# Optimization experiments

Hardware: AMD Instinct MI355X
Metric: run time of the kernel (lower is better)

The kernel has to match this reference:

```python
import jax, jax.numpy as jnp
import numpy as np

BIT = 64
NUM_TRAIN = 200000
BATCH = 256
NUM_CLASSES = 100
MAX_SAMPLE = 30          # max_SampleNum in original
ALPHA = 0.01             # config['alpha']
M = 2 * BIT              # self.m = 2 * bit


def setup_inputs() -> dict:
    key = jax.random.key(0)
    k1, k2, k3, k4, k5 = jax.random.split(key, 5)
    u = jax.random.normal(k1, (BATCH, BIT), dtype=jnp.float32)
    y = jax.random.randint(k2, (BATCH,), 0, NUM_CLASSES)
    # distinct scatter targets into the bank, like dataloader sample indices
    ind = jax.random.choice(k3, NUM_TRAIN, (BATCH,), replace=False)
    U = jax.random.normal(k4, (NUM_TRAIN, BIT), dtype=jnp.float32)
    Y = jax.random.randint(k5, (NUM_TRAIN,), 0, NUM_CLASSES).astype(jnp.float32)
    return {"u": u, "y": y, "ind": ind, "U": U, "Y": Y}


def reference(u, y, ind, U, Y):
    yf = y.astype(jnp.float32)
    # scatter update of the memory bank (u.data -> detached in original)
    U = U.at[ind].set(jax.lax.stop_gradient(u))
    Y = Y.at[ind].set(yf)

    # For each sample, the first MAX_SAMPLE ascending indices with Y == y[i]
    # (same as torch.where(self.Y == indx)[0][:max_SampleNum]).
    match = (Y[None, :] == yf[:, None])                       # (B, N)
    pos = jnp.arange(NUM_TRAIN, dtype=jnp.int32)
    # matched positions keep their index; unmatched get index + N -> sorted after
    key_mat = jnp.where(match, pos[None, :], pos[None, :] + NUM_TRAIN)  # (B, N)
    _, order = jax.lax.top_k(-key_mat, MAX_SAMPLE)            # (B, 30) ascending matched idx first
    count = jnp.minimum(match.sum(axis=1), MAX_SAMPLE)        # per-row pool size
    valid = (jnp.arange(MAX_SAMPLE)[None, :] < count[:, None]).reshape(-1)  # (B*30,)

    pool_idx = order.reshape(-1)                              # (P,) P = B*30
    U_pool = U[pool_idx]                                      # (P, bit)
    Y_pool = Y[pool_idx]                                      # (P,)

    # pairwise squared distance u vs pool
    dist = jnp.sum((u[:, None, :] - U_pool[None, :, :]) ** 2, axis=2)  # (B, P)
    mism = (yf[:, None] != Y_pool[None, :]).astype(jnp.float32)        # (B, P)
    pair = (1.0 - mism) * 0.5 * dist + mism * 0.5 * jnp.clip(M - dist, 0.0)

    vmask = valid.astype(jnp.float32)[None, :]
    step = jnp.sum(valid.astype(jnp.float32))                 # dynamic pool length in original
    loss1 = jnp.sum(pair * vmask) / (u.shape[0] * step)       # == loss.mean() over (B, step)
    loss2 = ALPHA * jnp.mean(jnp.abs(jnp.abs(u) - 1.0))
    return loss1 + loss2
```

## Files before the change

### kernel.cpp

```cpp
#include <hip/hip_runtime.h>

#define NTRAIN 200000
#define NB     256
#define BIT    64
#define MAXS   30
#define NCLS   100
#define ESPL   8
#define EPB    4
#define CHUNK  4096
#define PERT   16
#define NCLSB  (NCLS * ESPL)
#define MVAL   128.0f
#define ALPHA  0.01f

__global__ __launch_bounds__(256) void dsh_main_kernel(
    const float* __restrict__ u, const int* __restrict__ y,
    const int* __restrict__ ind, const float* __restrict__ U,
    const float* __restrict__ Y,
    float* __restrict__ partial, int* __restrict__ cntw)
{
    __shared__ int   addl[NB];
    __shared__ int   reml[NB];
    __shared__ float up_l[EPB * BIT];
    __shared__ int   pool[MAXS];
    __shared__ int   povr[EPB];
    __shared__ int   wsA[4], wsB[4], wsC[4];
    __shared__ float redf[4];

    const int t    = threadIdx.x;
    const int j    = blockIdx.x;
    const int lane = t & 63;
    const int wave = t >> 6;

    const int c = j >> 3;
    const int e = j & 7;
    const float cf = (float)c;

    const int myi = ind[t];
    const int myy = y[t];
    const int s0  = t * PERT;
    float4 yv0, yv1, yv2, yv3;
    {
        const float4* yp = (const float4*)(Y + s0);
        yv0 = yp[0]; yv1 = yp[1]; yv2 = yp[2]; yv3 = yp[3];
    }
    const float ybank = Y[myi];

    const bool ismem = (myy == c);
    const bool fneg  = ismem && (ybank != cf);
    const bool fpos  = (!ismem) && (ybank == cf);
    unsigned long long balm = __ballot(ismem);
    unsigned long long bala = __ballot(fneg);
    unsigned long long balr = __ballot(fpos);
    if (lane == 0) {
        wsA[wave] = (int)__popcll(balm);
        wsB[wave] = (int)__popcll(bala);
        wsC[wave] = (int)__popcll(balr);
    }
    __syncthreads();
    const int mult = wsA[0] + wsA[1] + wsA[2] + wsA[3];

    if (mult == 0) {
        if (t == 0) { partial[j] = 0.f; if (e == 0) cntw[c] = 0; }
        return;
    }

    const int nadd = wsB[0] + wsB[1] + wsB[2] + wsB[3];
    const int nrem = wsC[0] + wsC[1] + wsC[2] + wsC[3];
    int pa = 0, pr = 0;
    #pragma unroll
    for (int w = 0; w < 4; ++w) if (w < wave) { pa += wsB[w]; pr += wsC[w]; }
    const unsigned long long lm = (1ull << lane) - 1ull;
    if (fneg) addl[pa + (int)__popcll(bala & lm)] = myi;
    if (fpos) reml[pr + (int)__popcll(balr & lm)] = myi;
    __syncthreads();

    unsigned mbits = 0;
    if (yv0.x == cf) mbits |= 1u << 0;
    if (yv0.y == cf) mbits |= 1u << 1;
    if (yv0.z == cf) mbits |= 1u << 2;
    if (yv0.w == cf) mbits |= 1u << 3;
    if (yv1.x == cf) mbits |= 1u << 4;
    if (yv1.y == cf) mbits |= 1u << 5;
    if (yv1.z == cf) mbits |= 1u << 6;
    if (yv1.w == cf) mbits |= 1u << 7;
    if (yv2.x == cf) mbits |= 1u << 8;
    if (yv2.y == cf) mbits |= 1u << 9;
    if (yv2.z == cf) mbits |= 1u << 10;
    if (yv2.w == cf) mbits |= 1u << 11;
    if (yv3.x == cf) mbits |= 1u << 12;
    if (yv3.y == cf) mbits |= 1u << 13;
    if (yv3.z == cf) mbits |= 1u << 14;
    if (yv3.w == cf) mbits |= 1u << 15;
    for (int a2 = 0; a2 < nadd; ++a2) {
        unsigned rel = (unsigned)(addl[a2] - s0);
        if (rel < (unsigned)PERT) mbits |= 1u << rel;
    }
    for (int r2 = 0; r2 < nrem; ++r2) {
        unsigned rel = (unsigned)(reml[r2] - s0);
        if (rel < (unsigned)PERT) mbits &= ~(1u << rel);
    }
    const int mcnt = __popc(mbits);

    int x = mcnt;
    #pragma unroll
    for (int off = 1; off < 64; off <<= 1) {
        int v2 = __shfl_up(x, off, 64);
        if (lane >= off) x += v2;
    }
    if (lane == 63) wsA[wave] = x;
    if (t < EPB) povr[t] = -1;
    __syncthreads();
    int r = x - mcnt;
    #pragma unroll
    for (int w = 0; w < 4; ++w) if (w < wave) r += wsA[w];
    #pragma unroll
    for (int k = 0; k < PERT; ++k) {
        if ((mbits >> k) & 1u) {
            if (r < MAXS) pool[r] = s0 + k;
            ++r;
        }
    }
    int count = wsA[0] + wsA[1] + wsA[2] + wsA[3];
    __syncthreads();

    for (int base = CHUNK; base < NTRAIN && count < MAXS; base += CHUNK) {
        const int s = base + t * PERT;
        unsigned mb = 0;
        int mc = 0;
        if (s < NTRAIN) {
            const float4* yp = (const float4*)(Y + s);
            float4 a0 = yp[0], a1 = yp[1], a2v = yp[2], a3 = yp[3];
            if (a0.x == cf) mb |= 1u << 0;
            if (a0.y == cf) mb |= 1u << 1;
            if (a0.z == cf) mb |= 1u << 2;
            if (a0.w == cf) mb |= 1u << 3;
            if (a1.x == cf) mb |= 1u << 4;
            if (a1.y == cf) mb |= 1u << 5;
            if (a1.z == cf) mb |= 1u << 6;
            if (a1.w == cf) mb |= 1u << 7;
            if (a2v.x == cf) mb |= 1u << 8;
            if (a2v.y == cf) mb |= 1u << 9;
            if (a2v.z == cf) mb |= 1u << 10;
            if (a2v.w == cf) mb |= 1u << 11;
            if (a3.x == cf) mb |= 1u << 12;
            if (a3.y == cf) mb |= 1u << 13;
            if (a3.z == cf) mb |= 1u << 14;
            if (a3.w == cf) mb |= 1u << 15;
            for (int a2 = 0; a2 < nadd; ++a2) {
                unsigned rel = (unsigned)(addl[a2] - s);
                if (rel < (unsigned)PERT) mb |= 1u << rel;
            }
            for (int r2 = 0; r2 < nrem; ++r2) {
                unsigned rel = (unsigned)(reml[r2] - s);
                if (rel < (unsigned)PERT) mb &= ~(1u << rel);
            }
            mc = __popc(mb);
        }
        int xx = mc;
        #pragma unroll
        for (int off = 1; off < 64; off <<= 1) {
            int v2 = __shfl_up(xx, off, 64);
            if (lane >= off) xx += v2;
        }
        if (lane == 63) wsA[wave] = xx;
        __syncthreads();
        int rr = count + (xx - mc);
        #pragma unroll
        for (int w = 0; w < 4; ++w) if (w < wave) rr += wsA[w];
        #pragma unroll
        for (int k = 0; k < PERT; ++k) {
            if ((mb >> k) & 1u) {
                if (rr < MAXS) pool[rr] = s + k;
                ++rr;
            }
        }
        count += wsA[0] + wsA[1] + wsA[2] + wsA[3];
        __syncthreads();
    }
    const int cnt = (count < MAXS) ? count : MAXS;

    const int p0 = e * EPB;
    const int pe = (p0 + EPB < cnt) ? p0 + EPB : cnt;
    for (int k2 = p0; k2 < pe; ++k2)
        if (myi == pool[k2]) povr[k2 - p0] = t;
    __syncthreads();

    float4 ur[16];
    {
        const float4* urp = (const float4*)(u + t * BIT);
        #pragma unroll
        for (int q2 = 0; q2 < 16; ++q2) ur[q2] = urp[q2];
    }
    {
        const int pp = t >> 6;
        const int d  = t & 63;
        float v = 0.f;
        if (p0 + pp < pe) {
            const int ov = povr[pp];
            v = (ov >= 0) ? u[ov * BIT + d] : U[pool[p0 + pp] * BIT + d];
        }
        up_l[t] = v;
    }
    __syncthreads();

    const bool same = (myy == c);
    const int npool = pe - p0;
    float acc = 0.f;
    for (int pp = 0; pp < npool; ++pp) {
        const float4* up = (const float4*)(up_l + pp * BIT);
        float d0 = 0.f, d1 = 0.f, d2 = 0.f, d3 = 0.f;
        #pragma unroll
        for (int q2 = 0; q2 < 16; ++q2) {
            float4 v = up[q2];
            float a0 = ur[q2].x - v.x; d0 += a0 * a0;
            float a1 = ur[q2].y - v.y; d1 += a1 * a1;
            float a2 = ur[q2].z - v.z; d2 += a2 * a2;
            float a3 = ur[q2].w - v.w; d3 += a3 * a3;
        }
        const float dist = (d0 + d1) + (d2 + d3);
        acc += same ? dist : fmaxf(MVAL - dist, 0.f);
    }
    #pragma unroll
    for (int off = 32; off; off >>= 1) acc += __shfl_down(acc, off, 64);
    if (lane == 0) redf[wave] = acc;
    __syncthreads();
    if (t == 0) {
        partial[j] = (float)mult * (redf[0] + redf[1] + redf[2] + redf[3]);
        if (e == 0) cntw[c] = mult * cnt;
    }
}

__global__ __launch_bounds__(256) void dsh_final_kernel(
    const float* __restrict__ u,
    const float* __restrict__ partial, const int* __restrict__ cntw,
    float* __restrict__ out)
{
    const int t = threadIdx.x;
    const int lane = t & 63, wave = t >> 6;
    __shared__ float redp[4], reda[4];
    __shared__ int   redc[4];

    float p = partial[t] + partial[t + 256] + partial[t + 512];
    if (t < NCLSB - 768) p += partial[t + 768];
    int cc = (t < NCLS) ? cntw[t] : 0;

    float a = 0.f;
    #pragma unroll
    for (int k = 0; k < 16; ++k) {
        float4 v = ((const float4*)u)[t + 256 * k];
        a += fabsf(fabsf(v.x) - 1.f) + fabsf(fabsf(v.y) - 1.f)
           + fabsf(fabsf(v.z) - 1.f) + fabsf(fabsf(v.w) - 1.f);
    }
    #pragma unroll
    for (int off = 32; off; off >>= 1) {
        p  += __shfl_down(p,  off, 64);
        a  += __shfl_down(a,  off, 64);
        cc += __shfl_down(cc, off, 64);
    }
    if (lane == 0) { redp[wave] = p; reda[wave] = a; redc[wave] = cc; }
    __syncthreads();
    if (t == 0) {
        const float P = redp[0] + redp[1] + redp[2] + redp[3];
        const float A = reda[0] + reda[1] + reda[2] + reda[3];
        const int   S = redc[0] + redc[1] + redc[2] + redc[3];
        out[0] = 0.5f * P / (256.0f * (float)S)
               + ALPHA * (A * (1.0f / 16384.0f));
    }
}

extern "C" void kernel_launch(void* const* d_in, const int* in_sizes, int n_in,
                              void* d_out, int out_size, void* d_ws, size_t ws_size,
                              hipStream_t stream) {
    const float* u   = (const float*)d_in[0];
    const int*   y   = (const int*)d_in[1];
    const int*   ind = (const int*)d_in[2];
    const float* U   = (const float*)d_in[3];
    const float* Y   = (const float*)d_in[4];
    float* out = (float*)d_out;

    float* partial = (float*)d_ws;
    int*   cntw    = (int*)((char*)d_ws + 4096);

    dsh_main_kernel<<<dim3(NCLSB), dim3(256), 0, stream>>>(
        u, y, ind, U, Y, partial, cntw);
    dsh_final_kernel<<<dim3(1), dim3(256), 0, stream>>>(u, partial, cntw, out);
}
```

Before: 22.80 us.

## Fuse final reduction into main kernel via last-block atomic counters

Replaces the separate final reduction kernel with a last-block-done pattern. Each block stores its partial results, then bumps a two-level atomic counter (per-100-block octant, then a root), and the last block does the final reduction. A small prep kernel now launched before the main kernel resets the counters and computes the regularization sum, so that work leaves the serialized tail. The launch count stays at two. The intended saving is the tail latency of the single-block final kernel after the main grid. The cost is atomic traffic and relaxed memory ordering, which rests on an s_waitcnt and atomic reads for visibility.

```diff
diff --git a/kernel.cpp b/kernel.cpp
--- a/kernel.cpp
+++ b/kernel.cpp
@@ -5,19 +5,46 @@
 #define BIT    64
 #define MAXS   30
 #define NCLS   100
-#define ESPL   8
 #define EPB    4
 #define CHUNK  4096
 #define PERT   16
-#define NCLSB  (NCLS * ESPL)
+#define NCLSB  (NCLS * 8)
 #define MVAL   128.0f
 #define ALPHA  0.01f
+
+
+__global__ __launch_bounds__(256) void dsh_prep_kernel(
+    const float* __restrict__ u, int* __restrict__ oct, int* __restrict__ root,
+    float* __restrict__ regsum)
+{
+    const int t = threadIdx.x;
+    const int lane = t & 63, wave = t >> 6;
+    __shared__ float redf[4];
+
+    if (t < 8) oct[t] = 0;
+    if (t == 8) *root = 0;
+
+    float a = 0.f;
+    #pragma unroll
+    for (int k = 0; k < 16; ++k) {
+        float4 v = ((const float4*)u)[t + 256 * k];
+        a += fabsf(fabsf(v.x) - 1.f) + fabsf(fabsf(v.y) - 1.f)
+           + fabsf(fabsf(v.z) - 1.f) + fabsf(fabsf(v.w) - 1.f);
+    }
+    #pragma unroll
+    for (int off = 32; off; off >>= 1) a += __shfl_down(a, off, 64);
+    if (lane == 0) redf[wave] = a;
+    __syncthreads();
+    if (t == 0) *regsum = redf[0] + redf[1] + redf[2] + redf[3];
+}
 
 __global__ __launch_bounds__(256) void dsh_main_kernel(
     const float* __restrict__ u, const int* __restrict__ y,
     const int* __restrict__ ind, const float* __restrict__ U,
     const float* __restrict__ Y,
-    float* __restrict__ partial, int* __restrict__ cntw)
+    float* __restrict__ partial, int* __restrict__ cntw,
+    int* __restrict__ oct, int* __restrict__ root,
+    const float* __restrict__ regsum, float* __restrict__ out)
 {
     __shared__ int   addl[NB];
     __shared__ int   reml[NB];
@@ -25,7 +52,9 @@
     __shared__ int   pool[MAXS];
     __shared__ int   povr[EPB];
     __shared__ int   wsA[4], wsB[4], wsC[4];
-    __shared__ float redf[4];
+    __shared__ float redf[4], redg[4];
+    __shared__ int   redi[4];
+    __shared__ int   lastflag;
 
     const int t    = threadIdx.x;
     const int j    = blockIdx.x;
@@ -35,6 +64,9 @@
     const int c = j >> 3;
     const int e = j & 7;
     const float cf = (float)c;
+
+    float myPair = 0.f;
+    int   myCntW = (e == 0) ? 0 : -1;
 
     const int myi = ind[t];
     const int myy = y[t];
@@ -60,210 +92,217 @@
     __syncthreads();
     const int mult = wsA[0] + wsA[1] + wsA[2] + wsA[3];
 
-    if (mult == 0) {
-        if (t == 0) { partial[j] = 0.f; if (e == 0) cntw[c] = 0; }
-        return;
-    }
-
-    const int nadd = wsB[0] + wsB[1] + wsB[2] + wsB[3];
-    const int nrem = wsC[0] + wsC[1] + wsC[2] + wsC[3];
-    int pa = 0, pr = 0;
-    #pragma unroll
-    for (int w = 0; w < 4; ++w) if (w < wave) { pa += wsB[w]; pr += wsC[w]; }
-    const unsigned long long lm = (1ull << lane) - 1ull;
-    if (fneg) addl[pa + (int)__popcll(bala & lm)] = myi;
-    if (fpos) reml[pr + (int)__popcll(balr & lm)] = myi;
+    if (mult > 0) {
+        const int nadd = wsB[0] + wsB[1] + wsB[2] + wsB[3];
+        const int nrem = wsC[0] + wsC[1] + wsC[2] + wsC[3];
+        int pa = 0, pr = 0;
+        #pragma unroll
+        for (int w = 0; w < 4; ++w) if (w < wave) { pa += wsB[w]; pr += wsC[w]; }
+        const unsigned long long lm = (1ull << lane) - 1ull;
+        if (fneg) addl[pa + (int)__popcll(bala & lm)] = myi;
+        if (fpos) reml[pr + (int)__popcll(balr & lm)] = myi;
+        __syncthreads();
+
+        unsigned mbits = 0;
+        if (yv0.x == cf) mbits |= 1u << 0;
+        if (yv0.y == cf) mbits |= 1u << 1;
+        if (yv0.z == cf) mbits |= 1u << 2;
+        if (yv0.w == cf) mbits |= 1u << 3;
+        if (yv1.x == cf) mbits |= 1u << 4;
+        if (yv1.y == cf) mbits |= 1u << 5;
+        if (yv1.z == cf) mbits |= 1u << 6;
+        if (yv1.w == cf) mbits |= 1u << 7;
+        if (yv2.x == cf) mbits |= 1u << 8;
+        if (yv2.y == cf) mbits |= 1u << 9;
+        if (yv2.z == cf) mbits |= 1u << 10;
+        if (yv2.w == cf) mbits |= 1u << 11;
+        if (yv3.x == cf) mbits |= 1u << 12;
+        if (yv3.y == cf) mbits |= 1u << 13;
+        if (yv3.z == cf) mbits |= 1u << 14;
+        if (yv3.w == cf) mbits |= 1u << 15;
+        for (int a2 = 0; a2 < nadd; ++a2) {
+            unsigned rel = (unsigned)(addl[a2] - s0);
+            if (rel < (unsigned)PERT) mbits |= 1u << rel;
+        }
+        for (int r2 = 0; r2 < nrem; ++r2) {
+            unsigned rel = (unsigned)(reml[r2] - s0);
+            if (rel < (unsigned)PERT) mbits &= ~(1u << rel);
+        }
+        const int mcnt = __popc(mbits);
+
+        int x = mcnt;
+        #pragma unroll
+        for (int off = 1; off < 64; off <<= 1) {
+            int v2 = __shfl_up(x, off, 64);
+            if (lane >= off) x += v2;
+        }
+        if (lane == 63) wsA[wave] = x;
+        if (t < EPB) povr[t] = -1;
+        __syncthreads();
+        int r = x - mcnt;
+        #pragma unroll
+        for (int w = 0; w < 4; ++w) if (w < wave) r += wsA[w];
+        #pragma unroll
+        for (int k = 0; k < PERT; ++k) {
+            if ((mbits >> k) & 1u) {
+                if (r < MAXS) pool[r] = s0 + k;
+                ++r;
+            }
+        }
+        int count = wsA[0] + wsA[1] + wsA[2] + wsA[3];
+        __syncthreads();
+
+        for (int base = CHUNK; base < NTRAIN && count < MAXS; base += CHUNK) {
+            const int s = base + t * PERT;
+            unsigned mb = 0;
+            int mc = 0;
+            if (s < NTRAIN) {
+                const float4* yp = (const float4*)(Y + s);
+                float4 a0 = yp[0], a1 = yp[1], a2v = yp[2], a3 = yp[3];
+                if (a0.x == cf) mb |= 1u << 0;
+                if (a0.y == cf) mb |= 1u << 1;
+                if (a0.z == cf) mb |= 1u << 2;
+                if (a0.w == cf) mb |= 1u << 3;
+                if (a1.x == cf) mb |= 1u << 4;
+                if (a1.y == cf) mb |= 1u << 5;
+                if (a1.z == cf) mb |= 1u << 6;
+                if (a1.w == cf) mb |= 1u << 7;
+                if (a2v.x == cf) mb |= 1u << 8;
+                if (a2v.y == cf) mb |= 1u << 9;
+                if (a2v.z == cf) mb |= 1u << 10;
+                if (a2v.w == cf) mb |= 1u << 11;
+                if (a3.x == cf) mb |= 1u << 12;
+                if (a3.y == cf) mb |= 1u << 13;
+                if (a3.z == cf) mb |= 1u << 14;
+                if (a3.w == cf) mb |= 1u << 15;
+                for (int a2 = 0; a2 < nadd; ++a2) {
+                    unsigned rel = (unsigned)(addl[a2] - s);
+                    if (rel < (unsigned)PERT) mb |= 1u << rel;
+                }
+                for (int r2 = 0; r2 < nrem; ++r2) {
+                    unsigned rel = (unsigned)(reml[r2] - s);
+                    if (rel < (unsigned)PERT) mb &= ~(1u << rel);
+                }
+                mc = __popc(mb);
+            }
+            int xx = mc;
+            #pragma unroll
+            for (int off = 1; off < 64; off <<= 1) {
+                int v2 = __shfl_up(xx, off, 64);
+                if (lane >= off) xx += v2;
+            }
+            if (lane == 63) wsA[wave] = xx;
+            __syncthreads();
+            int rr = count + (xx - mc);
+            #pragma unroll
+            for (int w = 0; w < 4; ++w) if (w < wave) rr += wsA[w];
+            #pragma unroll
+            for (int k = 0; k < PERT; ++k) {
+                if ((mb >> k) & 1u) {
+                    if (rr < MAXS) pool[rr] = s + k;
+                    ++rr;
+                }
+            }
+            count += wsA[0] + wsA[1] + wsA[2] + wsA[3];
+            __syncthreads();
+        }
+        const int cnt = (count < MAXS) ? count : MAXS;
+
+        const int p0 = e * EPB;
+        const int pe = (p0 + EPB < cnt) ? p0 + EPB : cnt;
+        for (int k2 = p0; k2 < pe; ++k2)
+            if (myi == pool[k2]) povr[k2 - p0] = t;
+        __syncthreads();
+
+        float4 ur[16];
+        {
+            const float4* urp = (const float4*)(u + t * BIT);
+            #pragma unroll
+            for (int q2 = 0; q2 < 16; ++q2) ur[q2] = urp[q2];
+        }
+        {
+            const int pp = t >> 6;
+            const int d  = t & 63;
+            float v = 0.f;
+            if (p0 + pp < pe) {
+                const int ov = povr[pp];
+                v = (ov >= 0) ? u[ov * BIT + d] : U[pool[p0 + pp] * BIT + d];
+            }
+            up_l[t] = v;
+        }
+        __syncthreads();
+
+        const bool same = (myy == c);
+        const int npool = pe - p0;
+        float acc = 0.f;
+        for (int pp = 0; pp < npool; ++pp) {
+            const float4* up = (const float4*)(up_l + pp * BIT);
+            float d0 = 0.f, d1 = 0.f, d2 = 0.f, d3 = 0.f;
+            #pragma unroll
+            for (int q2 = 0; q2 < 16; ++q2) {
+                float4 v = up[q2];
+                float a0 = ur[q2].x - v.x; d0 += a0 * a0;
+                float a1 = ur[q2].y - v.y; d1 += a1 * a1;
+                float a2 = ur[q2].z - v.z; d2 += a2 * a2;
+                float a3 = ur[q2].w - v.w; d3 += a3 * a3;
+            }
+            const float dist = (d0 + d1) + (d2 + d3);
+            acc += same ? dist : fmaxf(MVAL - dist, 0.f);
+        }
+        #pragma unroll
+        for (int off = 32; off; off >>= 1) acc += __shfl_down(acc, off, 64);
+        if (lane == 0) redf[wave] = acc;
+        __syncthreads();
+        if (t == 0) {
+            myPair = (float)mult * (redf[0] + redf[1] + redf[2] + redf[3]);
+            if (e == 0) myCntW = mult * cnt;
+        }
+    }
+
+    if (t == 0) {
+        __hip_atomic_store(&partial[j], myPair, __ATOMIC_RELAXED,
+                           __HIP_MEMORY_SCOPE_AGENT);
+        if (myCntW >= 0)
+            __hip_atomic_store(&cntw[c], myCntW, __ATOMIC_RELAXED,
+                               __HIP_MEMORY_SCOPE_AGENT);
+        asm volatile("s_waitcnt vmcnt(0)" ::: "memory");
+        int isLast = 0;
+        int oo = __hip_atomic_fetch_add(&oct[j / 100], 1, __ATOMIC_RELAXED,
+                                        __HIP_MEMORY_SCOPE_AGENT);
+        if (oo == 99) {
+            int ro = __hip_atomic_fetch_add(root, 1, __ATOMIC_RELAXED,
+                                            __HIP_MEMORY_SCOPE_AGENT);
+            isLast = (ro == 7);
+        }
+        lastflag = isLast;
+    }
     __syncthreads();
-
-    unsigned mbits = 0;
-    if (yv0.x == cf) mbits |= 1u << 0;
-    if (yv0.y == cf) mbits |= 1u << 1;
-    if (yv0.z == cf) mbits |= 1u << 2;
-    if (yv0.w == cf) mbits |= 1u << 3;
-    if (yv1.x == cf) mbits |= 1u << 4;
-    if (yv1.y == cf) mbits |= 1u << 5;
-    if (yv1.z == cf) mbits |= 1u << 6;
-    if (yv1.w == cf) mbits |= 1u << 7;
-    if (yv2.x == cf) mbits |= 1u << 8;
-    if (yv2.y == cf) mbits |= 1u << 9;
-    if (yv2.z == cf) mbits |= 1u << 10;
-    if (yv2.w == cf) mbits |= 1u << 11;
-    if (yv3.x == cf) mbits |= 1u << 12;
-    if (yv3.y == cf) mbits |= 1u << 13;
-    if (yv3.z == cf) mbits |= 1u << 14;
-    if (yv3.w == cf) mbits |= 1u << 15;
-    for (int a2 = 0; a2 < nadd; ++a2) {
-        unsigned rel = (unsigned)(addl[a2] - s0);
-        if (rel < (unsigned)PERT) mbits |= 1u << rel;
-    }
-    for (int r2 = 0; r2 < nrem; ++r2) {
-        unsigned rel = (unsigned)(reml[r2] - s0);
-        if (rel < (unsigned)PERT) mbits &= ~(1u << rel);
-    }
-    const int mcnt = __popc(mbits);
-
-    int x = mcnt;
-    #pragma unroll
-    for (int off = 1; off < 64; off <<= 1) {
-        int v2 = __shfl_up(x, off, 64);
-        if (lane >= off) x += v2;
-    }
-    if (lane == 63) wsA[wave] = x;
-    if (t < EPB) povr[t] = -1;
-    __syncthreads();
-    int r = x - mcnt;
-    #pragma unroll
-    for (int w = 0; w < 4; ++w) if (w < wave) r += wsA[w];
-    #pragma unroll
-    for (int k = 0; k < PERT; ++k) {
-        if ((mbits >> k) & 1u) {
-            if (r < MAXS) pool[r] = s0 + k;
-            ++r;
-        }
-    }
-    int count = wsA[0] + wsA[1] + wsA[2] + wsA[3];
-    __syncthreads();
-
-    for (int base = CHUNK; base < NTRAIN && count < MAXS; base += CHUNK) {
-        const int s = base + t * PERT;
-        unsigned mb = 0;
-        int mc = 0;
-        if (s < NTRAIN) {
-            const float4* yp = (const float4*)(Y + s);
-            float4 a0 = yp[0], a1 = yp[1], a2v = yp[2], a3 = yp[3];
-            if (a0.x == cf) mb |= 1u << 0;
-            if (a0.y == cf) mb |= 1u << 1;
-            if (a0.z == cf) mb |= 1u << 2;
-            if (a0.w == cf) mb |= 1u << 3;
-            if (a1.x == cf) mb |= 1u << 4;
-            if (a1.y == cf) mb |= 1u << 5;
-            if (a1.z == cf) mb |= 1u << 6;
-            if (a1.w == cf) mb |= 1u << 7;
-            if (a2v.x == cf) mb |= 1u << 8;
-            if (a2v.y == cf) mb |= 1u << 9;
-            if (a2v.z == cf) mb |= 1u << 10;
-            if (a2v.w == cf) mb |= 1u << 11;
-            if (a3.x == cf) mb |= 1u << 12;
-            if (a3.y == cf) mb |= 1u << 13;
-            if (a3.z == cf) mb |= 1u << 14;
-            if (a3.w == cf) mb |= 1u << 15;
-            for (int a2 = 0; a2 < nadd; ++a2) {
-                unsigned rel = (unsigned)(addl[a2] - s);
-                if (rel < (unsigned)PERT) mb |= 1u << rel;
-            }
-            for (int r2 = 0; r2 < nrem; ++r2) {
-                unsigned rel = (unsigned)(reml[r2] - s);
-                if (rel < (unsigned)PERT) mb &= ~(1u << rel);
-            }
-            mc = __popc(mb);
-        }
-        int xx = mc;
-        #pragma unroll
-        for (int off = 1; off < 64; off <<= 1) {
-            int v2 = __shfl_up(xx, off, 64);
-            if (lane >= off) xx += v2;
-        }
-        if (lane == 63) wsA[wave] = xx;
-        __syncthreads();
-        int rr = count + (xx - mc);
-        #pragma unroll
-        for (int w = 0; w < 4; ++w) if (w < wave) rr += wsA[w];
-        #pragma unroll
-        for (int k = 0; k < PERT; ++k) {
-            if ((mb >> k) & 1u) {
-                if (rr < MAXS) pool[rr] = s + k;
-                ++rr;
-            }
-        }
-        count += wsA[0] + wsA[1] + wsA[2] + wsA[3];
-        __syncthreads();
-    }
-    const int cnt = (count < MAXS) ? count : MAXS;
-
-    const int p0 = e * EPB;
-    const int pe = (p0 + EPB < cnt) ? p0 + EPB : cnt;
-    for (int k2 = p0; k2 < pe; ++k2)
-        if (myi == pool[k2]) povr[k2 - p0] = t;
-    __syncthreads();
-
-    float4 ur[16];
-    {
-        const float4* urp = (const float4*)(u + t * BIT);
-        #pragma unroll
-        for (int q2 = 0; q2 < 16; ++q2) ur[q2] = urp[q2];
-    }
-    {
-        const int pp = t >> 6;
-        const int d  = t & 63;
-        float v = 0.f;
-        if (p0 + pp < pe) {
-            const int ov = povr[pp];
-            v = (ov >= 0) ? u[ov * BIT + d] : U[pool[p0 + pp] * BIT + d];
-        }
-        up_l[t] = v;
-    }
-    __syncthreads();
-
-    const bool same = (myy == c);
-    const int npool = pe - p0;
-    float acc = 0.f;
-    for (int pp = 0; pp < npool; ++pp) {
-        const float4* up = (const float4*)(up_l + pp * BIT);
-        float d0 = 0.f, d1 = 0.f, d2 = 0.f, d3 = 0.f;
-        #pragma unroll
-        for (int q2 = 0; q2 < 16; ++q2) {
-            float4 v = up[q2];
-            float a0 = ur[q2].x - v.x; d0 += a0 * a0;
-            float a1 = ur[q2].y - v.y; d1 += a1 * a1;
-            float a2 = ur[q2].z - v.z; d2 += a2 * a2;
-            float a3 = ur[q2].w - v.w; d3 += a3 * a3;
-        }
-        const float dist = (d0 + d1) + (d2 + d3);
-        acc += same ? dist : fmaxf(MVAL - dist, 0.f);
-    }
-    #pragma unroll
-    for (int off = 32; off; off >>= 1) acc += __shfl_down(acc, off, 64);
-    if (lane == 0) redf[wave] = acc;
-    __syncthreads();
-    if (t == 0) {
-        partial[j] = (float)mult * (redf[0] + redf[1] + redf[2] + redf[3]);
-        if (e == 0) cntw[c] = mult * cnt;
-    }
-}
-
-__global__ __launch_bounds__(256) void dsh_final_kernel(
-    const float* __restrict__ u,
-    const float* __restrict__ partial, const int* __restrict__ cntw,
-    float* __restrict__ out)
-{
-    const int t = threadIdx.x;
-    const int lane = t & 63, wave = t >> 6;
-    __shared__ float redp[4], reda[4];
-    __shared__ int   redc[4];
-
-    float p = partial[t] + partial[t + 256] + partial[t + 512];
-    if (t < NCLSB - 768) p += partial[t + 768];
-    int cc = (t < NCLS) ? cntw[t] : 0;
-
-    float a = 0.f;
-    #pragma unroll
-    for (int k = 0; k < 16; ++k) {
-        float4 v = ((const float4*)u)[t + 256 * k];
-        a += fabsf(fabsf(v.x) - 1.f) + fabsf(fabsf(v.y) - 1.f)
-           + fabsf(fabsf(v.z) - 1.f) + fabsf(fabsf(v.w) - 1.f);
-    }
+    if (!lastflag) return;
+
+    float p = __hip_atomic_fetch_add(&partial[t], 0.f, __ATOMIC_RELAXED,
+                                     __HIP_MEMORY_SCOPE_AGENT)
+            + __hip_atomic_fetch_add(&partial[t + 256], 0.f, __ATOMIC_RELAXED,
+                                     __HIP_MEMORY_SCOPE_AGENT)
+            + __hip_atomic_fetch_add(&partial[t + 512], 0.f, __ATOMIC_RELAXED,
+                                     __HIP_MEMORY_SCOPE_AGENT);
+    if (t < NCLSB - 768)
+        p += __hip_atomic_fetch_add(&partial[t + 768], 0.f, __ATOMIC_RELAXED,
+                                    __HIP_MEMORY_SCOPE_AGENT);
+    int cc = (t < NCLS)
+           ? __hip_atomic_fetch_add(&cntw[t], 0, __ATOMIC_RELAXED,
+                                    __HIP_MEMORY_SCOPE_AGENT)
+           : 0;
     #pragma unroll
     for (int off = 32; off; off >>= 1) {
         p  += __shfl_down(p,  off, 64);
-        a  += __shfl_down(a,  off, 64);
         cc += __shfl_down(cc, off, 64);
     }
-    if (lane == 0) { redp[wave] = p; reda[wave] = a; redc[wave] = cc; }
+    if (lane == 0) { redg[wave] = p; redi[wave] = cc; }
     __syncthreads();
     if (t == 0) {
-        const float P = redp[0] + redp[1] + redp[2] + redp[3];
-        const float A = reda[0] + reda[1] + reda[2] + reda[3];
-        const int   S = redc[0] + redc[1] + redc[2] + redc[3];
+        const float P = redg[0] + redg[1] + redg[2] + redg[3];
+        const int   S = redi[0] + redi[1] + redi[2] + redi[3];
+        const float A = *regsum;
         out[0] = 0.5f * P / (256.0f * (float)S)
                + ALPHA * (A * (1.0f / 16384.0f));
     }
@@ -281,8 +320,11 @@
 
     float* partial = (float*)d_ws;
     int*   cntw    = (int*)((char*)d_ws + 4096);
-
+    int*   oct     = (int*)((char*)d_ws + 8192);
+    int*   root    = (int*)((char*)d_ws + 8224);
+    float* regsum  = (float*)((char*)d_ws + 8240);
+
+    dsh_prep_kernel<<<dim3(1), dim3(256), 0, stream>>>(u, oct, root, regsum);
     dsh_main_kernel<<<dim3(NCLSB), dim3(256), 0, stream>>>(
-        u, y, ind, U, Y, partial, cntw);
-    dsh_final_kernel<<<dim3(1), dim3(256), 0, stream>>>(u, partial, cntw, out);
+        u, y, ind, U, Y, partial, cntw, oct, root, regsum, out);
 }
```

Result: slower. 31.83 us (+39.6%).

## Split class scan from pair distance into separate kernels with atomic bins

Applied to the files above, without the earlier changes.

The scan for matching pool indices now runs once per class instead of being repeated by all 8 sub-blocks of each class. A new pair kernel launches 3200 small 64-thread blocks, each computing distances for 4 pool entries against 64 rows, and accumulates results into strided atomic bins. The |u| regulariser is moved into extra blocks of the scan kernel. This removes the 8x redundant Y scanning but adds a third kernel launch and atomics, and reads pool rows from global memory rather than shared memory.

```diff
diff --git a/kernel.cpp b/kernel.cpp
--- a/kernel.cpp
+++ b/kernel.cpp
@@ -5,25 +5,35 @@
 #define BIT    64
 #define MAXS   30
 #define NCLS   100
-#define ESPL   8
-#define EPB    4
 #define CHUNK  4096
 #define PERT   16
-#define NCLSB  (NCLS * ESPL)
+#define NREG   16
 #define MVAL   128.0f
 #define ALPHA  0.01f
 
-__global__ __launch_bounds__(256) void dsh_main_kernel(
+#define NBIN   128
+#define BSTR   16
+#define PAIRB  (NCLS * 32)
+
+struct Ws {
+    int   pool[NCLS][32];
+    int   povr[NCLS][32];
+    int   cnt[NCLS];
+    int   mult[NCLS];
+    int   cntw[NCLS];
+    float regp[NREG];
+    float bins[NBIN * BSTR];
+};
+
+__global__ __launch_bounds__(256) void dsh_scan_kernel(
     const float* __restrict__ u, const int* __restrict__ y,
-    const int* __restrict__ ind, const float* __restrict__ U,
-    const float* __restrict__ Y,
-    float* __restrict__ partial, int* __restrict__ cntw)
+    const int* __restrict__ ind, const float* __restrict__ Y,
+    Ws* __restrict__ ws)
 {
     __shared__ int   addl[NB];
     __shared__ int   reml[NB];
-    __shared__ float up_l[EPB * BIT];
     __shared__ int   pool[MAXS];
-    __shared__ int   povr[EPB];
+    __shared__ int   povr[MAXS];
     __shared__ int   wsA[4], wsB[4], wsC[4];
     __shared__ float redf[4];
 
@@ -32,8 +42,24 @@
     const int lane = t & 63;
     const int wave = t >> 6;
 
-    const int c = j >> 3;
-    const int e = j & 7;
+    if (j >= NCLS + NREG) {
+        if (t < NBIN) ws->bins[t * BSTR] = 0.f;
+        return;
+    }
+    if (j >= NCLS) {
+        const int q = j - NCLS;
+        float4 v = ((const float4*)u)[q * 256 + t];
+        float a = fabsf(fabsf(v.x) - 1.f) + fabsf(fabsf(v.y) - 1.f)
+                + fabsf(fabsf(v.z) - 1.f) + fabsf(fabsf(v.w) - 1.f);
+        #pragma unroll
+        for (int off = 32; off; off >>= 1) a += __shfl_down(a, off, 64);
+        if (lane == 0) redf[wave] = a;
+        __syncthreads();
+        if (t == 0) ws->regp[q] = redf[0] + redf[1] + redf[2] + redf[3];
+        return;
+    }
+
+    const int c = j;
     const float cf = (float)c;
 
     const int myi = ind[t];
@@ -59,12 +85,10 @@
     }
     __syncthreads();
     const int mult = wsA[0] + wsA[1] + wsA[2] + wsA[3];
-
     if (mult == 0) {
-        if (t == 0) { partial[j] = 0.f; if (e == 0) cntw[c] = 0; }
+        if (t == 0) { ws->cnt[c] = 0; ws->mult[c] = 0; ws->cntw[c] = 0; }
         return;
     }
-
     const int nadd = wsB[0] + wsB[1] + wsB[2] + wsB[3];
     const int nrem = wsC[0] + wsC[1] + wsC[2] + wsC[3];
     int pa = 0, pr = 0;
@@ -109,7 +133,7 @@
         if (lane >= off) x += v2;
     }
     if (lane == 63) wsA[wave] = x;
-    if (t < EPB) povr[t] = -1;
+    if (t < MAXS) povr[t] = -1;
     __syncthreads();
     int r = x - mcnt;
     #pragma unroll
@@ -180,78 +204,83 @@
     }
     const int cnt = (count < MAXS) ? count : MAXS;
 
-    const int p0 = e * EPB;
-    const int pe = (p0 + EPB < cnt) ? p0 + EPB : cnt;
-    for (int k2 = p0; k2 < pe; ++k2)
-        if (myi == pool[k2]) povr[k2 - p0] = t;
-    __syncthreads();
+    for (int k = 0; k < cnt; ++k)
+        if (myi == pool[k]) povr[k] = t;
+    __syncthreads();
+    if (t < MAXS) {
+        ws->pool[c][t] = (t < cnt) ? pool[t] : 0;
+        ws->povr[c][t] = (t < cnt) ? povr[t] : -1;
+    }
+    if (t == 0) {
+        ws->cnt[c]  = cnt;
+        ws->mult[c] = mult;
+        ws->cntw[c] = mult * cnt;
+    }
+}
+
+__global__ __launch_bounds__(64) void dsh_pair_kernel(
+    const float* __restrict__ u, const int* __restrict__ y,
+    const float* __restrict__ U, Ws* __restrict__ ws)
+{
+    const int t  = threadIdx.x;
+    const int j  = blockIdx.x;
+    const int c  = j >> 5;
+    const int e  = (j >> 2) & 7;
+    const int rq = j & 3;
+
+    const int mult = ws->mult[c];
+    if (mult == 0) return;
+    const int cnt = ws->cnt[c];
+    const int p0  = e * 4;
+    if (p0 >= cnt) return;
+    const int pe  = (p0 + 4 < cnt) ? p0 + 4 : cnt;
+
+    const int i = rq * 64 + t;
+    const bool same = (y[i] == c);
 
     float4 ur[16];
     {
-        const float4* urp = (const float4*)(u + t * BIT);
-        #pragma unroll
-        for (int q2 = 0; q2 < 16; ++q2) ur[q2] = urp[q2];
-    }
-    {
-        const int pp = t >> 6;
-        const int d  = t & 63;
-        float v = 0.f;
-        if (p0 + pp < pe) {
-            const int ov = povr[pp];
-            v = (ov >= 0) ? u[ov * BIT + d] : U[pool[p0 + pp] * BIT + d];
-        }
-        up_l[t] = v;
-    }
-    __syncthreads();
-
-    const bool same = (myy == c);
-    const int npool = pe - p0;
+        const float4* urp = (const float4*)(u + i * BIT);
+        #pragma unroll
+        for (int q = 0; q < 16; ++q) ur[q] = urp[q];
+    }
+
     float acc = 0.f;
-    for (int pp = 0; pp < npool; ++pp) {
-        const float4* up = (const float4*)(up_l + pp * BIT);
+    for (int p = p0; p < pe; ++p) {
+        const int ov = ws->povr[c][p];
+        const int bi = ws->pool[c][p];
+        const float4* rp = (ov >= 0) ? (const float4*)(u + ov * BIT)
+                                     : (const float4*)(U + bi * BIT);
         float d0 = 0.f, d1 = 0.f, d2 = 0.f, d3 = 0.f;
         #pragma unroll
-        for (int q2 = 0; q2 < 16; ++q2) {
-            float4 v = up[q2];
-            float a0 = ur[q2].x - v.x; d0 += a0 * a0;
-            float a1 = ur[q2].y - v.y; d1 += a1 * a1;
-            float a2 = ur[q2].z - v.z; d2 += a2 * a2;
-            float a3 = ur[q2].w - v.w; d3 += a3 * a3;
+        for (int q = 0; q < 16; ++q) {
+            float4 v = rp[q];
+            float a0 = ur[q].x - v.x; d0 += a0 * a0;
+            float a1 = ur[q].y - v.y; d1 += a1 * a1;
+            float a2 = ur[q].z - v.z; d2 += a2 * a2;
+            float a3 = ur[q].w - v.w; d3 += a3 * a3;
         }
         const float dist = (d0 + d1) + (d2 + d3);
         acc += same ? dist : fmaxf(MVAL - dist, 0.f);
     }
+
     #pragma unroll
     for (int off = 32; off; off >>= 1) acc += __shfl_down(acc, off, 64);
-    if (lane == 0) redf[wave] = acc;
-    __syncthreads();
-    if (t == 0) {
-        partial[j] = (float)mult * (redf[0] + redf[1] + redf[2] + redf[3]);
-        if (e == 0) cntw[c] = mult * cnt;
-    }
+    if (t == 0)
+        atomicAdd(&ws->bins[(j & (NBIN - 1)) * BSTR], (float)mult * acc);
 }
 
-__global__ __launch_bounds__(256) void dsh_final_kernel(
-    const float* __restrict__ u,
-    const float* __restrict__ partial, const int* __restrict__ cntw,
-    float* __restrict__ out)
+__global__ __launch_bounds__(256) void dsh_reduce_kernel(
+    Ws* __restrict__ ws, float* __restrict__ out)
 {
     const int t = threadIdx.x;
     const int lane = t & 63, wave = t >> 6;
     __shared__ float redp[4], reda[4];
     __shared__ int   redc[4];
 
-    float p = partial[t] + partial[t + 256] + partial[t + 512];
-    if (t < NCLSB - 768) p += partial[t + 768];
-    int cc = (t < NCLS) ? cntw[t] : 0;
-
-    float a = 0.f;
-    #pragma unroll
-    for (int k = 0; k < 16; ++k) {
-        float4 v = ((const float4*)u)[t + 256 * k];
-        a += fabsf(fabsf(v.x) - 1.f) + fabsf(fabsf(v.y) - 1.f)
-           + fabsf(fabsf(v.z) - 1.f) + fabsf(fabsf(v.w) - 1.f);
-    }
+    float p = (t < NBIN) ? ws->bins[t * BSTR] : 0.f;
+    float a = (t < NREG) ? ws->regp[t] : 0.f;
+    int  cc = (t < NCLS) ? ws->cntw[t] : 0;
     #pragma unroll
     for (int off = 32; off; off >>= 1) {
         p  += __shfl_down(p,  off, 64);
@@ -278,11 +307,9 @@
     const float* U   = (const float*)d_in[3];
     const float* Y   = (const float*)d_in[4];
     float* out = (float*)d_out;
-
-    float* partial = (float*)d_ws;
-    int*   cntw    = (int*)((char*)d_ws + 4096);
-
-    dsh_main_kernel<<<dim3(NCLSB), dim3(256), 0, stream>>>(
-        u, y, ind, U, Y, partial, cntw);
-    dsh_final_kernel<<<dim3(1), dim3(256), 0, stream>>>(u, partial, cntw, out);
+    Ws*    ws  = (Ws*)d_ws;
+
+    dsh_scan_kernel<<<dim3(NCLS + NREG + 1), dim3(256), 0, stream>>>(u, y, ind, Y, ws);
+    dsh_pair_kernel<<<dim3(PAIRB), dim3(64), 0, stream>>>(u, y, U, ws);
+    dsh_reduce_kernel<<<dim3(1), dim3(256), 0, stream>>>(ws, out);
 }
```

Measured after the change: 23.43 us. 2.7% more time.
